# Optimization experiments

Hardware: AMD Instinct MI355X
Metric: run time of the kernel (lower is better)

The kernel has to match this reference:

```python
import jax, jax.numpy as jnp
import numpy as np

B, N_HEADS, D_MODEL, S = 4, 16, 128, 2048
SQRT_D = np.sqrt(D_MODEL).astype(np.float32)


def setup_inputs() -> dict:
    key = jax.random.key(0)
    kx, kq, kk, kv, kw = jax.random.split(key, 5)
    N = B * N_HEADS
    return {
        "x": jax.random.normal(kx, (B, D_MODEL, S), dtype=jnp.float32),
        "Q": jax.random.normal(kq, (N, D_MODEL, S), dtype=jnp.float32),
        "K": jax.random.normal(kk, (N, D_MODEL, S), dtype=jnp.float32),
        "V": jax.random.normal(kv, (N, D_MODEL, S), dtype=jnp.float32),
        "W": jax.random.normal(kw, (N_HEADS * D_MODEL, D_MODEL), dtype=jnp.float32) * 0.02,
    }


def reference(x, Q, K, V, W):
    # x contributes only its shape (the repeated copy is overwritten in the original)
    b, d_model, s = x.shape
    # scores[n, i, j] = sum_d Q[n, d, i] * K[n, d, j] / sqrt(d_model)
    scores = jnp.einsum("ndi,ndj->nij", Q, K) / SQRT_D  # [N, S, S]
    # legacy F.softmax (no dim) on a 3D tensor -> softmax over dim=1 (query index)
    attn = jax.nn.softmax(scores, axis=1)
    # out[n, d, j] = sum_i V[n, d, i] * attn[n, i, j]
    out = jnp.einsum("ndi,nij->ndj", V, attn)  # [N, d_model, S]
    out = out.reshape(b, N_HEADS * d_model, s)  # [B, H*d_model, S]
    # final projection: W^T @ out, W: [H*d_model, d_model]
    return jnp.einsum("hd,bhs->bds", W, out)  # [B, d_model, S]
```

## Files before the change

kernel.cpp:

```cpp
#include <hip/hip_runtime.h>
#include <hip/hip_bf16.h>

typedef unsigned short u16;
typedef unsigned int   u32;
typedef short  short8v __attribute__((ext_vector_type(8)));
typedef u16    u16x8   __attribute__((ext_vector_type(8)));
typedef float  f32x16  __attribute__((ext_vector_type(16)));
typedef float  f32x4v  __attribute__((ext_vector_type(4)));
typedef u32    u32x2   __attribute__((ext_vector_type(2)));
typedef u32    u32x4   __attribute__((ext_vector_type(4)));

#define HEADS 64
#define DMODEL 128
#define SEQ 2048


__device__ __forceinline__ f32x16 mfma_bf16(short8v a, short8v b, f32x16 c) {
  return __builtin_amdgcn_mfma_f32_32x32x16_bf16(a, b, c, 0, 0, 0);
}

__device__ __forceinline__ f32x16 fzero16() {
  f32x16 z;
#pragma unroll
  for (int i = 0; i < 16; ++i) z[i] = 0.f;
  return z;
}

__device__ __forceinline__ float fast_exp2(float x) {
  float r;
  asm("v_exp_f32 %0, %1" : "=v"(r) : "v"(x));
  return r;
}

__device__ __forceinline__ u32 bfround(float x) {
  u32 u = __builtin_bit_cast(u32, x);
  u += 0x7fffu + ((u >> 16) & 1u);
  return u >> 16;
}
__device__ __forceinline__ u32 bfpair(float lo, float hi) {
  u32 a = __builtin_bit_cast(u32, lo); a += 0x7fffu + ((a >> 16) & 1u);
  u32 b = __builtin_bit_cast(u32, hi); b += 0x7fffu + ((b >> 16) & 1u);
  return (a >> 16) | (b & 0xffff0000u);
}
__device__ __forceinline__ u32 packbf(float lo, float hi) {
  u32 l16 = (u32)__builtin_bit_cast(u16, __float2bfloat16(lo));
  u32 h16 = (u32)__builtin_bit_cast(u16, __float2bfloat16(hi));
  return l16 | (h16 << 16);
}

typedef const __attribute__((address_space(1))) void* gp1_t;
typedef __attribute__((address_space(3))) void* lp3_t;
__device__ __forceinline__ void gload16(const u16* g, u16* l) {
  __builtin_amdgcn_global_load_lds((gp1_t)g, (lp3_t)l, 16, 0, 0);
}

#define PIPE_BARRIER()                                        \
  do {                                                        \
    asm volatile("s_waitcnt vmcnt(4)" ::: "memory");          \
    __builtin_amdgcn_sched_barrier(0);                        \
    __builtin_amdgcn_s_barrier();                             \
    __builtin_amdgcn_sched_barrier(0);                        \
  } while (0)

__device__ __forceinline__ void stage_T(const float* __restrict__ src, int pos0,
                                        u16* lds, int tid) {
  int ic = tid & 7;
  int d0 = (tid >> 3) * 2;
  const float* p = src + d0 * SEQ + pos0 + ic * 8;
  f32x4v xa = *reinterpret_cast<const f32x4v*>(p);
  f32x4v xb = *reinterpret_cast<const f32x4v*>(p + 4);
  f32x4v ya = *reinterpret_cast<const f32x4v*>(p + SEQ);
  f32x4v yb = *reinterpret_cast<const f32x4v*>(p + SEQ + 4);
  u32* lds32 = reinterpret_cast<u32*>(lds);
  int cc = d0 >> 3;
#pragma unroll
  for (int k = 0; k < 8; ++k) {
    int r = ic * 8 + k;
    int c2 = cc ^ (r & 15);
    float xv = (k < 4) ? xa[k & 3] : xb[k & 3];
    float yv = (k < 4) ? ya[k & 3] : yb[k & 3];
    lds32[(r * 128 + c2 * 8 + (d0 & 7)) >> 1] = bfpair(xv, yv);
  }
}

__device__ __forceinline__ short8v ld_at(const u16* lds, int row, int chunk) {
  return *reinterpret_cast<const short8v*>(lds + row * 128 + ((chunk ^ (row & 15)) * 8));
}
__device__ __forceinline__ short8v ld_vt(const u16* lds, int d, int chunk) {
  return *reinterpret_cast<const short8v*>(lds + d * 64 + ((chunk ^ (d & 7)) * 8));
}


__global__ __launch_bounds__(256) void prep_qt(const float* __restrict__ Q,
                                               u16* __restrict__ Qt) {
  int blk = blockIdx.x;
  int n = blk >> 5, pt = blk & 31;
  const float* src = Q + (size_t)n * DMODEL * SEQ;
  u16* dst = Qt + (size_t)n * SEQ * DMODEL + (size_t)pt * 64 * DMODEL;
  int t = threadIdx.x;
  int pq = t & 15, dq = t >> 4;
#pragma unroll
  for (int p = 0; p < 2; ++p) {
    int d0 = (dq + 16 * p) * 4;
    const float* s0 = src + (size_t)d0 * SEQ + pt * 64 + pq * 4;
    f32x4v r0 = *reinterpret_cast<const f32x4v*>(s0);
    f32x4v r1 = *reinterpret_cast<const f32x4v*>(s0 + SEQ);
    f32x4v r2 = *reinterpret_cast<const f32x4v*>(s0 + 2 * SEQ);
    f32x4v r3 = *reinterpret_cast<const f32x4v*>(s0 + 3 * SEQ);
#pragma unroll
    for (int j = 0; j < 4; ++j) {
      u32x2 v = { bfpair(r0[j], r1[j]), bfpair(r2[j], r3[j]) };
      *reinterpret_cast<u32x2*>(dst + (pq * 4 + j) * DMODEL + d0) = v;
    }
  }
}

__global__ __launch_bounds__(256) void prep_v(const float* __restrict__ V,
                                              u16* __restrict__ V16t) {
  int blk = blockIdx.x;
  int n = blk >> 5, it = blk & 31;
  int t = threadIdx.x;
  int s8 = (t & 7) * 8;
  const float* src = V + (size_t)n * DMODEL * SEQ + it * 64 + s8;
  u16* dst = V16t + (size_t)blk * DMODEL * 64 + s8;
#pragma unroll
  for (int rr = 0; rr < 4; ++rr) {
    int d = (t >> 3) + 32 * rr;
    const float* p = src + (size_t)d * SEQ;
    f32x4v a = *reinterpret_cast<const f32x4v*>(p);
    f32x4v b = *reinterpret_cast<const f32x4v*>(p + 4);
    u32x4 v = { bfpair(a[0], a[1]), bfpair(a[2], a[3]),
                bfpair(b[0], b[1]), bfpair(b[2], b[3]) };
    *reinterpret_cast<u32x4*>(dst + d * 64) = v;
  }
}

__global__ void wtrans_kernel(const float* __restrict__ Wsrc, u16* __restrict__ Wt) {
  int e = blockIdx.x * 256 + threadIdx.x;
#pragma unroll
  for (int rr = 0; rr < 2; ++rr) {
    int o = e + rr * 131072;
    int dm = o >> 11, c = o & 2047;
    Wt[o] = (u16)bfround(Wsrc[c * 128 + dm]);
  }
}

#define BUFW (64 * 128 + 128 * 64)

__global__ __launch_bounds__(512, 2) void attn_kernel(
    const u16* __restrict__ Qt, const float* __restrict__ K,
    const u16* __restrict__ V16t, u16* __restrict__ Ows) {
  __shared__ __align__(16) u16 LDSb[3 * BUFW];
  const int tid = threadIdx.x;
  const int w = tid >> 6;
  const int lane = tid & 63;
  const int g = lane >> 5;
  const int lj = lane & 31;
  const int p_ = blockIdx.x;
  const int n = ((p_ >> 6) << 3) | (p_ & 7);
  const int j0 = ((p_ >> 3) & 7) * 256;
  const u16* Qtn = Qt + (size_t)n * SEQ * DMODEL;
  const float* Kb = K + (size_t)n * DMODEL * SEQ;
  const u16* Vtn = V16t + (size_t)n * 32 * DMODEL * 64;

  int qoff[4], voff[4];
#pragma unroll
  for (int i = 0; i < 4; ++i) {
    int idx = (w & 3) * 4 + i;
    int pos = idx * 4 + (lane >> 4);
    qoff[i] = pos * DMODEL + (((lane & 15) ^ (pos & 15)) * 8);
    int d = idx * 8 + (lane >> 3);
    voff[i] = d * 64 + (((lane & 7) ^ (d & 7)) * 8);
  }

#define ISSUE_TILE(tile, buf)                                              \
  {                                                                        \
    if (w < 4) {                                                           \
      const u16* qb = Qtn + (size_t)(tile) * (64 * DMODEL);                \
      _Pragma("unroll") for (int i = 0; i < 4; ++i)                        \
          gload16(qb + qoff[i], (buf) + ((w & 3) * 4 + i) * 512);          \
    } else {                                                               \
      const u16* vb = Vtn + (size_t)(tile) * (DMODEL * 64);                \
      _Pragma("unroll") for (int i = 0; i < 4; ++i)                        \
          gload16(vb + voff[i], (buf) + 64 * DMODEL + ((w & 3) * 4 + i) * 512); \
    }                                                                      \
  }

  ISSUE_TILE(0, LDSb);
  ISSUE_TILE(1, LDSb + BUFW);

  short8v bq[8];
  u16* KS = LDSb + 2 * BUFW;
#pragma unroll 1
  for (int p = 0; p < 4; ++p) {
    stage_T(Kb, j0 + p * 64, KS, tid);
    __syncthreads();
    if ((w >> 1) == p) {
      int row = (w & 1) * 32 + lj;
#pragma unroll
      for (int c = 0; c < 8; ++c) bq[c] = ld_at(KS, row, 2 * c + g);
    }
    __syncthreads();
  }

  f32x16 o0 = fzero16(), o1 = fzero16(), o2 = fzero16(), o3 = fzero16();
  float m_run = -1e30f, l_run = 0.f;
  const float SC = (float)(1.4426950408889634 / 11.313708498984761);

  int cidx = 0;
#pragma unroll 1
  for (int ib = 0; ib < 32; ++ib) {
    u16* curAT = LDSb + cidx * BUFW;
    u16* curVT = curAT + 64 * DMODEL;
    int widx = cidx + 2; if (widx >= 3) widx -= 3;
    u16* nxt = LDSb + widx * BUFW;
    cidx = (cidx >= 2) ? 0 : cidx + 1;

    ISSUE_TILE((ib + 2) & 31, nxt);

    f32x16 c0 = fzero16(), c1 = fzero16();
    __builtin_amdgcn_s_setprio(1);
#pragma unroll
    for (int dc = 0; dc < 8; ++dc) {
      short8v a0 = ld_at(curAT, lj, 2 * dc + g);
      short8v a1 = ld_at(curAT, 32 + lj, 2 * dc + g);
      c0 = mfma_bf16(a0, bq[dc], c0);
      c1 = mfma_bf16(a1, bq[dc], c1);
    }
    __builtin_amdgcn_s_setprio(0);

    float mx = -1e30f;
#pragma unroll
    for (int r = 0; r < 16; ++r) { c0[r] *= SC; mx = fmaxf(mx, c0[r]); }
#pragma unroll
    for (int r = 0; r < 16; ++r) { c1[r] *= SC; mx = fmaxf(mx, c1[r]); }
    mx = fmaxf(mx, __shfl_xor(mx, 32, 64));

    if (!__all(mx <= m_run + 8.f)) {
      float mn = fmaxf(m_run, mx);
      float al = fast_exp2(m_run - mn);
      m_run = mn;
      l_run *= al;
#pragma unroll
      for (int r = 0; r < 16; ++r) { o0[r] *= al; o1[r] *= al; o2[r] *= al; o3[r] *= al; }
    }
    float ps = 0.f;
#pragma unroll
    for (int r = 0; r < 16; ++r) { c0[r] = fast_exp2(c0[r] - m_run); ps += c0[r]; }
#pragma unroll
    for (int r = 0; r < 16; ++r) { c1[r] = fast_exp2(c1[r] - m_run); ps += c1[r]; }
    ps += __shfl_xor(ps, 32, 64);
    l_run += ps;

    u32 pk[8], ok[8];
#pragma unroll
    for (int half = 0; half < 2; ++half) {
#pragma unroll
      for (int q = 0; q < 4; ++q) {
#pragma unroll
        for (int h = 0; h < 2; ++h) {
          float va = half ? c1[q * 4 + 2 * h]     : c0[q * 4 + 2 * h];
          float vb = half ? c1[q * 4 + 2 * h + 1] : c0[q * 4 + 2 * h + 1];
          pk[q * 2 + h] = packbf(va, vb);
        }
      }
#pragma unroll
      for (int i = 0; i < 8; ++i) ok[i] = __shfl_xor(pk[i], 32, 64);
      __builtin_amdgcn_s_setprio(1);
#pragma unroll
      for (int kh = 0; kh < 2; ++kh) {
        int kc = half * 2 + kh;
        const int base = 4 * kh;
        u32 w0 = g ? ok[base + 2] : pk[base + 0];
        u32 w1 = g ? ok[base + 3] : pk[base + 1];
        u32 w2 = g ? pk[base + 2] : ok[base + 0];
        u32 w3 = g ? pk[base + 3] : ok[base + 1];
        u32x4 uu = {w0, w1, w2, w3};
        short8v pf = __builtin_bit_cast(short8v, uu);
        short8v v0 = ld_vt(curVT, lj,      2 * kc + g);
        short8v v1 = ld_vt(curVT, 32 + lj, 2 * kc + g);
        short8v v2 = ld_vt(curVT, 64 + lj, 2 * kc + g);
        short8v v3 = ld_vt(curVT, 96 + lj, 2 * kc + g);
        o0 = mfma_bf16(v0, pf, o0);
        o1 = mfma_bf16(v1, pf, o1);
        o2 = mfma_bf16(v2, pf, o2);
        o3 = mfma_bf16(v3, pf, o3);
      }
      __builtin_amdgcn_s_setprio(0);
    }
    PIPE_BARRIER();
  }

  float inv = 1.f / l_run;
  int jme = j0 + w * 32 + lj;
  u16* obase = Ows + ((size_t)n * SEQ + jme) * DMODEL;

#define STORE_OT(OV, DT)                                                  \
  {                                                                       \
    _Pragma("unroll") for (int q = 0; q < 4; ++q) {                       \
      int d0 = (DT) * 32 + 4 * g + 8 * q;                                 \
      u32x2 val;                                                          \
      val.x = bfpair(OV[4 * q + 0] * inv, OV[4 * q + 1] * inv);           \
      val.y = bfpair(OV[4 * q + 2] * inv, OV[4 * q + 3] * inv);           \
      *reinterpret_cast<u32x2*>(obase + d0) = val;                        \
    }                                                                     \
  }
  STORE_OT(o0, 0) STORE_OT(o1, 1) STORE_OT(o2, 2) STORE_OT(o3, 3)
#undef STORE_OT
#undef ISSUE_TILE
}

__global__ __launch_bounds__(256) void proj_kernel(
    const u16* __restrict__ Ows, const u16* __restrict__ Wt, float* __restrict__ out) {
  __shared__ __align__(16) u16 BT[32 * 128];
  const int tid = threadIdx.x;
  const int w = tid >> 6, lane = tid & 63, g = lane >> 5, lj = lane & 31;
  const int b = blockIdx.x >> 6;
  const int j0 = (blockIdx.x & 63) * 32;
  f32x16 acc = fzero16();
#pragma unroll 1
  for (int h = 0; h < 16; ++h) {
    __syncthreads();
#pragma unroll
    for (int rr = 0; rr < 2; ++rr) {
      int s = tid + rr * 256;
      int r = s >> 4, cc = s & 15;
      u16x8 v = *reinterpret_cast<const u16x8*>(
          Ows + ((size_t)(b * 16 + h) * SEQ + j0 + r) * DMODEL + cc * 8);
      *reinterpret_cast<u16x8*>(BT + r * 128 + ((cc ^ (r & 7)) * 8)) = v;
    }
    __syncthreads();
#pragma unroll
    for (int kc = 0; kc < 8; ++kc) {
      short8v a = *reinterpret_cast<const short8v*>(
          Wt + (size_t)(w * 32 + lj) * SEQ + h * 128 + kc * 16 + g * 8);
      short8v bb = *reinterpret_cast<const short8v*>(
          BT + lj * 128 + (((2 * kc + g) ^ (lj & 7)) * 8));
      acc = mfma_bf16(a, bb, acc);
    }
  }
#pragma unroll
  for (int q = 0; q < 4; ++q) {
#pragma unroll
    for (int r = 0; r < 4; ++r) {
      int dm = w * 32 + 4 * g + 8 * q + r;
      out[((size_t)b * DMODEL + dm) * SEQ + j0 + lj] = acc[4 * q + r];
    }
  }
}

extern "C" void kernel_launch(void* const* d_in, const int* in_sizes, int n_in,
                              void* d_out, int out_size, void* d_ws, size_t ws_size,
                              hipStream_t stream) {
  (void)in_sizes; (void)n_in; (void)out_size; (void)ws_size;
  const float* Q = (const float*)d_in[1];
  const float* K = (const float*)d_in[2];
  const float* V = (const float*)d_in[3];
  const float* W = (const float*)d_in[4];
  const size_t NEL = (size_t)HEADS * SEQ * DMODEL;
  u16* Qt   = (u16*)d_ws;
  u16* V16t = Qt + NEL;
  u16* Ows  = V16t + NEL;
  u16* Wt   = Ows + NEL;
  float* out = (float*)d_out;

  prep_qt<<<dim3(2048), dim3(256), 0, stream>>>(Q, Qt);
  prep_v<<<dim3(2048), dim3(256), 0, stream>>>(V, V16t);
  wtrans_kernel<<<dim3(512), dim3(256), 0, stream>>>(W, Wt);
  attn_kernel<<<dim3(512), dim3(512), 0, stream>>>(Qt, K, V16t, Ows);
  proj_kernel<<<dim3(256), dim3(256), 0, stream>>>(Ows, Wt, out);
}
```

Measured before the change: 248.0 us.

## Fold softmax scale into Q prep and process two KV tiles per barrier

Pre-scales Q by log2(e)/sqrt(d) during the bf16 transpose so the attention loop no longer multiplies scores. The attention loop now double-buffers pairs of Q/V tiles in four LDS slots, issuing the next pair's loads and syncing once per two tiles instead of once per tile. Max and sum reductions use tree form to shorten dependency chains. It uses more LDS and waits on all outstanding loads each step, which may expose latency.

Result: faster. 243.1 us (-2.0%).

```diff
diff --git a/kernel.cpp b/kernel.cpp
--- a/kernel.cpp
+++ b/kernel.cpp
@@ -14,6 +14,8 @@
 #define DMODEL 128
 #define SEQ 2048
 
+#define SCQ 0.1275293f
+
 
 __device__ __forceinline__ f32x16 mfma_bf16(short8v a, short8v b, f32x16 c) {
   return __builtin_amdgcn_mfma_f32_32x32x16_bf16(a, b, c, 0, 0, 0);
@@ -53,14 +55,6 @@
 __device__ __forceinline__ void gload16(const u16* g, u16* l) {
   __builtin_amdgcn_global_load_lds((gp1_t)g, (lp3_t)l, 16, 0, 0);
 }
-
-#define PIPE_BARRIER()                                        \
-  do {                                                        \
-    asm volatile("s_waitcnt vmcnt(4)" ::: "memory");          \
-    __builtin_amdgcn_sched_barrier(0);                        \
-    __builtin_amdgcn_s_barrier();                             \
-    __builtin_amdgcn_sched_barrier(0);                        \
-  } while (0)
 
 __device__ __forceinline__ void stage_T(const float* __restrict__ src, int pos0,
                                         u16* lds, int tid) {
@@ -109,7 +103,7 @@
     f32x4v r3 = *reinterpret_cast<const f32x4v*>(s0 + 3 * SEQ);
 #pragma unroll
     for (int j = 0; j < 4; ++j) {
-      u32x2 v = { bfpair(r0[j], r1[j]), bfpair(r2[j], r3[j]) };
+      u32x2 v = { bfpair(r0[j] * SCQ, r1[j] * SCQ), bfpair(r2[j] * SCQ, r3[j] * SCQ) };
       *reinterpret_cast<u32x2*>(dst + (pq * 4 + j) * DMODEL + d0) = v;
     }
   }
@@ -150,7 +144,7 @@
 __global__ __launch_bounds__(512, 2) void attn_kernel(
     const u16* __restrict__ Qt, const float* __restrict__ K,
     const u16* __restrict__ V16t, u16* __restrict__ Ows) {
-  __shared__ __align__(16) u16 LDSb[3 * BUFW];
+  __shared__ __align__(16) u16 LDSb[4 * BUFW];
   const int tid = threadIdx.x;
   const int w = tid >> 6;
   const int lane = tid & 63;
@@ -186,109 +180,123 @@
     }                                                                      \
   }
 
-  ISSUE_TILE(0, LDSb);
-  ISSUE_TILE(1, LDSb + BUFW);
-
   short8v bq[8];
-  u16* KS = LDSb + 2 * BUFW;
 #pragma unroll 1
   for (int p = 0; p < 4; ++p) {
-    stage_T(Kb, j0 + p * 64, KS, tid);
+    stage_T(Kb, j0 + p * 64, LDSb, tid);
     __syncthreads();
     if ((w >> 1) == p) {
       int row = (w & 1) * 32 + lj;
 #pragma unroll
-      for (int c = 0; c < 8; ++c) bq[c] = ld_at(KS, row, 2 * c + g);
+      for (int c = 0; c < 8; ++c) bq[c] = ld_at(LDSb, row, 2 * c + g);
     }
     __syncthreads();
   }
+
+  ISSUE_TILE(0, LDSb);
+  ISSUE_TILE(1, LDSb + BUFW);
+  asm volatile("s_waitcnt vmcnt(0)" ::: "memory");
+  __builtin_amdgcn_s_barrier();
 
   f32x16 o0 = fzero16(), o1 = fzero16(), o2 = fzero16(), o3 = fzero16();
   float m_run = -1e30f, l_run = 0.f;
-  const float SC = (float)(1.4426950408889634 / 11.313708498984761);
-
-  int cidx = 0;
+
 #pragma unroll 1
-  for (int ib = 0; ib < 32; ++ib) {
-    u16* curAT = LDSb + cidx * BUFW;
-    u16* curVT = curAT + 64 * DMODEL;
-    int widx = cidx + 2; if (widx >= 3) widx -= 3;
-    u16* nxt = LDSb + widx * BUFW;
-    cidx = (cidx >= 2) ? 0 : cidx + 1;
-
-    ISSUE_TILE((ib + 2) & 31, nxt);
-
-    f32x16 c0 = fzero16(), c1 = fzero16();
-    __builtin_amdgcn_s_setprio(1);
-#pragma unroll
-    for (int dc = 0; dc < 8; ++dc) {
-      short8v a0 = ld_at(curAT, lj, 2 * dc + g);
-      short8v a1 = ld_at(curAT, 32 + lj, 2 * dc + g);
-      c0 = mfma_bf16(a0, bq[dc], c0);
-      c1 = mfma_bf16(a1, bq[dc], c1);
-    }
-    __builtin_amdgcn_s_setprio(0);
-
-    float mx = -1e30f;
-#pragma unroll
-    for (int r = 0; r < 16; ++r) { c0[r] *= SC; mx = fmaxf(mx, c0[r]); }
-#pragma unroll
-    for (int r = 0; r < 16; ++r) { c1[r] *= SC; mx = fmaxf(mx, c1[r]); }
-    mx = fmaxf(mx, __shfl_xor(mx, 32, 64));
-
-    if (!__all(mx <= m_run + 8.f)) {
-      float mn = fmaxf(m_run, mx);
-      float al = fast_exp2(m_run - mn);
-      m_run = mn;
-      l_run *= al;
-#pragma unroll
-      for (int r = 0; r < 16; ++r) { o0[r] *= al; o1[r] *= al; o2[r] *= al; o3[r] *= al; }
-    }
-    float ps = 0.f;
-#pragma unroll
-    for (int r = 0; r < 16; ++r) { c0[r] = fast_exp2(c0[r] - m_run); ps += c0[r]; }
-#pragma unroll
-    for (int r = 0; r < 16; ++r) { c1[r] = fast_exp2(c1[r] - m_run); ps += c1[r]; }
-    ps += __shfl_xor(ps, 32, 64);
-    l_run += ps;
-
-    u32 pk[8], ok[8];
-#pragma unroll
-    for (int half = 0; half < 2; ++half) {
-#pragma unroll
-      for (int q = 0; q < 4; ++q) {
-#pragma unroll
-        for (int h = 0; h < 2; ++h) {
-          float va = half ? c1[q * 4 + 2 * h]     : c0[q * 4 + 2 * h];
-          float vb = half ? c1[q * 4 + 2 * h + 1] : c0[q * 4 + 2 * h + 1];
-          pk[q * 2 + h] = packbf(va, vb);
-        }
-      }
-#pragma unroll
-      for (int i = 0; i < 8; ++i) ok[i] = __shfl_xor(pk[i], 32, 64);
+  for (int ss = 0; ss < 16; ++ss) {
+    u16* cp = LDSb + (ss & 1) * (2 * BUFW);
+    u16* op = LDSb + ((ss & 1) ^ 1) * (2 * BUFW);
+
+    ISSUE_TILE((2 * ss + 2) & 31, op);
+    ISSUE_TILE((2 * ss + 3) & 31, op + BUFW);
+
+#pragma unroll
+    for (int h = 0; h < 2; ++h) {
+      u16* curAT = cp + h * BUFW;
+      u16* curVT = curAT + 64 * DMODEL;
+
+      f32x16 c0 = fzero16(), c1 = fzero16();
       __builtin_amdgcn_s_setprio(1);
 #pragma unroll
-      for (int kh = 0; kh < 2; ++kh) {
-        int kc = half * 2 + kh;
-        const int base = 4 * kh;
-        u32 w0 = g ? ok[base + 2] : pk[base + 0];
-        u32 w1 = g ? ok[base + 3] : pk[base + 1];
-        u32 w2 = g ? pk[base + 2] : ok[base + 0];
-        u32 w3 = g ? pk[base + 3] : ok[base + 1];
-        u32x4 uu = {w0, w1, w2, w3};
-        short8v pf = __builtin_bit_cast(short8v, uu);
-        short8v v0 = ld_vt(curVT, lj,      2 * kc + g);
-        short8v v1 = ld_vt(curVT, 32 + lj, 2 * kc + g);
-        short8v v2 = ld_vt(curVT, 64 + lj, 2 * kc + g);
-        short8v v3 = ld_vt(curVT, 96 + lj, 2 * kc + g);
-        o0 = mfma_bf16(v0, pf, o0);
-        o1 = mfma_bf16(v1, pf, o1);
-        o2 = mfma_bf16(v2, pf, o2);
-        o3 = mfma_bf16(v3, pf, o3);
+      for (int dc = 0; dc < 8; ++dc) {
+        short8v a0 = ld_at(curAT, lj, 2 * dc + g);
+        short8v a1 = ld_at(curAT, 32 + lj, 2 * dc + g);
+        c0 = mfma_bf16(a0, bq[dc], c0);
+        c1 = mfma_bf16(a1, bq[dc], c1);
       }
       __builtin_amdgcn_s_setprio(0);
-    }
-    PIPE_BARRIER();
+
+      float m8[8];
+#pragma unroll
+      for (int r = 0; r < 8; ++r)
+        m8[r] = fmaxf(fmaxf(c0[r], c0[r + 8]), fmaxf(c1[r], c1[r + 8]));
+#pragma unroll
+      for (int r = 0; r < 4; ++r) m8[r] = fmaxf(m8[r], m8[r + 4]);
+      float mx = fmaxf(fmaxf(m8[0], m8[1]), fmaxf(m8[2], m8[3]));
+      mx = fmaxf(mx, __shfl_xor(mx, 32, 64));
+
+      if (!__all(mx <= m_run + 8.f)) {
+        float mn = fmaxf(m_run, mx);
+        float al = fast_exp2(m_run - mn);
+        m_run = mn;
+        l_run *= al;
+#pragma unroll
+        for (int r = 0; r < 16; ++r) { o0[r] *= al; o1[r] *= al; o2[r] *= al; o3[r] *= al; }
+      }
+#pragma unroll
+      for (int r = 0; r < 16; ++r) c0[r] = fast_exp2(c0[r] - m_run);
+#pragma unroll
+      for (int r = 0; r < 16; ++r) c1[r] = fast_exp2(c1[r] - m_run);
+      float s8[8];
+#pragma unroll
+      for (int r = 0; r < 8; ++r) s8[r] = (c0[r] + c0[r + 8]) + (c1[r] + c1[r + 8]);
+#pragma unroll
+      for (int r = 0; r < 4; ++r) s8[r] += s8[r + 4];
+      float ps = (s8[0] + s8[1]) + (s8[2] + s8[3]);
+      ps += __shfl_xor(ps, 32, 64);
+      l_run += ps;
+
+      u32 pk[8], ok[8];
+#pragma unroll
+      for (int half = 0; half < 2; ++half) {
+#pragma unroll
+        for (int q = 0; q < 4; ++q) {
+#pragma unroll
+          for (int hh = 0; hh < 2; ++hh) {
+            float va = half ? c1[q * 4 + 2 * hh]     : c0[q * 4 + 2 * hh];
+            float vb = half ? c1[q * 4 + 2 * hh + 1] : c0[q * 4 + 2 * hh + 1];
+            pk[q * 2 + hh] = packbf(va, vb);
+          }
+        }
+#pragma unroll
+        for (int i = 0; i < 8; ++i) ok[i] = __shfl_xor(pk[i], 32, 64);
+        __builtin_amdgcn_s_setprio(1);
+#pragma unroll
+        for (int kh = 0; kh < 2; ++kh) {
+          int kc = half * 2 + kh;
+          const int base = 4 * kh;
+          u32 w0 = g ? ok[base + 2] : pk[base + 0];
+          u32 w1 = g ? ok[base + 3] : pk[base + 1];
+          u32 w2 = g ? pk[base + 2] : ok[base + 0];
+          u32 w3 = g ? pk[base + 3] : ok[base + 1];
+          u32x4 uu = {w0, w1, w2, w3};
+          short8v pf = __builtin_bit_cast(short8v, uu);
+          short8v v0 = ld_vt(curVT, lj,      2 * kc + g);
+          short8v v1 = ld_vt(curVT, 32 + lj, 2 * kc + g);
+          short8v v2 = ld_vt(curVT, 64 + lj, 2 * kc + g);
+          short8v v3 = ld_vt(curVT, 96 + lj, 2 * kc + g);
+          o0 = mfma_bf16(v0, pf, o0);
+          o1 = mfma_bf16(v1, pf, o1);
+          o2 = mfma_bf16(v2, pf, o2);
+          o3 = mfma_bf16(v3, pf, o3);
+        }
+        __builtin_amdgcn_s_setprio(0);
+      }
+    }
+
+    asm volatile("s_waitcnt vmcnt(0)" ::: "memory");
+    __builtin_amdgcn_sched_barrier(0);
+    __builtin_amdgcn_s_barrier();
+    __builtin_amdgcn_sched_barrier(0);
   }
 
   float inv = 1.f / l_run;
```
